# Optimization experiments

Hardware: AMD Instinct MI355X
Metric: run time of the kernel (lower is better)

Reference implementation:

```python
import jax, jax.numpy as jnp
import numpy as np

HEADS = 4
EPS = 1e-12

N_NODES = 50000
N_EDGES = 400000
N_GRAPHS = 512
IN_F = 70
HID = 128
N_LAYERS = 3
N_RELS = 86


def setup_inputs() -> dict:
    key = jax.random.key(0)
    ks = iter(jax.random.split(key, 32))
    inp = {}
    inp['h_x'] = jax.random.normal(next(ks), (N_NODES, IN_F), dtype=jnp.float32)
    inp['h_edge_index'] = jax.random.randint(next(ks), (2, N_EDGES), 0, N_NODES)
    inp['h_batch'] = jnp.sort(jax.random.randint(next(ks), (N_NODES,), 0, N_GRAPHS))
    inp['t_x'] = jax.random.normal(next(ks), (N_NODES, IN_F), dtype=jnp.float32)
    inp['t_edge_index'] = jax.random.randint(next(ks), (2, N_EDGES), 0, N_NODES)
    inp['t_batch'] = jnp.sort(jax.random.randint(next(ks), (N_NODES,), 0, N_GRAPHS))
    inp['rels'] = jax.random.randint(next(ks), (N_GRAPHS,), 0, N_RELS)
    # params
    s = 0.05
    inp['lin0_W'] = jax.random.normal(next(ks), (IN_F, HID), dtype=jnp.float32) * s
    inp['lin0_b'] = jnp.zeros((HID,), dtype=jnp.float32)
    # TransformerConv: lin_query/key/value map HID -> HEADS*HID; lin_skip HID->HID
    inp['Wq'] = jax.random.normal(next(ks), (N_LAYERS, HID, HEADS * HID), dtype=jnp.float32) * s
    inp['bq'] = jnp.zeros((N_LAYERS, HEADS * HID), dtype=jnp.float32)
    inp['Wk'] = jax.random.normal(next(ks), (N_LAYERS, HID, HEADS * HID), dtype=jnp.float32) * s
    inp['bk'] = jnp.zeros((N_LAYERS, HEADS * HID), dtype=jnp.float32)
    inp['Wv'] = jax.random.normal(next(ks), (N_LAYERS, HID, HEADS * HID), dtype=jnp.float32) * s
    inp['bv'] = jnp.zeros((N_LAYERS, HEADS * HID), dtype=jnp.float32)
    inp['Ws'] = jax.random.normal(next(ks), (N_LAYERS, HID, HID), dtype=jnp.float32) * s
    inp['bs'] = jnp.zeros((N_LAYERS, HID), dtype=jnp.float32)
    # cross attention
    inp['wq_W'] = jax.random.normal(next(ks), (HID, HID), dtype=jnp.float32) * s
    inp['wq_b'] = jnp.zeros((HID,), dtype=jnp.float32)
    inp['wk_W'] = jax.random.normal(next(ks), (HID, HID), dtype=jnp.float32) * s
    inp['wk_b'] = jnp.zeros((HID,), dtype=jnp.float32)
    # relation embedding (xavier-ish)
    inp['rel_emb'] = jax.random.normal(next(ks), (N_RELS, HID * HID), dtype=jnp.float32) * (1.0 / np.sqrt(HID))
    return inp


def _transformer_conv(x, src, dst, Wq, bq, Wk, bk, Wv, bv, Ws, bs):
    # PyG TransformerConv, heads=HEADS, concat=False (mean over heads), root skip.
    N = x.shape[0]
    D = Wq.shape[1] // HEADS  # per-head dim = out_channels
    q = (x @ Wq + bq).reshape(N, HEADS, D)
    k = (x @ Wk + bk).reshape(N, HEADS, D)
    v = (x @ Wv + bv).reshape(N, HEADS, D)
    scale = 1.0 / np.sqrt(D).astype(np.float32)
    alpha = jnp.einsum('ehd,ehd->eh', q[dst], k[src]) * scale  # [E,H]
    m = jax.ops.segment_max(alpha, dst, num_segments=N)        # per-dst max
    e = jnp.exp(alpha - m[dst])
    denom = jax.ops.segment_sum(e, dst, num_segments=N)
    a = e / denom[dst]                                          # segment softmax
    out = jax.ops.segment_sum(a[..., None] * v[src], dst, num_segments=N)  # [N,H,D]
    return out.mean(axis=1) + x @ Ws + bs


def _encode(x, edge_index, batch, lin0_W, lin0_b, Wq, bq, Wk, bk, Wv, bv, Ws, bs):
    src, dst = edge_index[0], edge_index[1]
    h = x @ lin0_W + lin0_b  # (dropout is a no-op in eval mode)
    for l in range(N_LAYERS):
        h = jax.nn.relu(_transformer_conv(h, src, dst, Wq[l], bq[l], Wk[l], bk[l], Wv[l], bv[l], Ws[l], bs[l]))
    return jax.ops.segment_sum(h, batch, num_segments=N_GRAPHS)  # global_add_pool [B,HID]


def _normalize(x, axis=-1):
    n = jnp.linalg.norm(x, axis=axis, keepdims=True)
    return x / jnp.maximum(n, EPS)


def reference(h_x, h_edge_index, h_batch, t_x, t_edge_index, t_batch, rels,
              lin0_W, lin0_b, Wq, bq, Wk, bk, Wv, bv, Ws, bs,
              wq_W, wq_b, wk_W, wk_b, rel_emb):
    h_embed = _encode(h_x, h_edge_index, h_batch, lin0_W, lin0_b, Wq, bq, Wk, bk, Wv, bv, Ws, bs)
    t_embed = _encode(t_x, t_edge_index, t_batch, lin0_W, lin0_b, Wq, bq, Wk, bk, Wv, bv, Ws, bs)
    # CrossDrugAttention
    q = h_embed @ wq_W + wq_b
    k = t_embed @ wk_W + wk_b
    interaction = jnp.tanh(q * k)
    # RelationalGeometryWarp
    rel_mat = _normalize(rel_emb[rels].reshape(-1, HID, HID))        # [B,F,F]
    h = _normalize(h_embed + interaction)                            # [B,F]
    t = _normalize(t_embed + interaction)                            # [B,F]
    score = jnp.einsum('bi,bij,bj->b', h, rel_mat, t)
    return score
```

## Files before the change

kernel.cpp:

```cpp
#include <hip/hip_runtime.h>
#include <math.h>

#define HID 128

typedef __attribute__((ext_vector_type(8))) short short8;
typedef __attribute__((ext_vector_type(4))) float f32x4;
typedef __attribute__((ext_vector_type(2))) float f32x2;

__device__ __forceinline__ float bf2f(unsigned int u16) {
  union { unsigned int i; float f; } x; x.i = u16 << 16; return x.f;
}
__device__ __forceinline__ unsigned short f2bf(float f) {
  union { float f; unsigned int i; } x; x.f = f;
  unsigned int i = x.i;
  unsigned int r = i + 0x7FFFu + ((i >> 16) & 1u);
  return (unsigned short)(r >> 16);
}

__device__ __forceinline__ unsigned char f2fp8_sw(float f) {
  union { float f; unsigned int u; } v; v.f = f;
  unsigned int s = (v.u >> 24) & 0x80u;
  v.u &= 0x7FFFFFFFu;
  if (v.f != v.f) return (unsigned char)(s | 0x7Fu);
  if (v.f >= 464.f) return (unsigned char)(s | 0x7Eu);
  if (v.f < 0.0009765625f) return (unsigned char)s;
  int ebits = (int)(v.u >> 23);
  if (ebits >= 121) {
    unsigned int r = v.u + 0x7FFFFu + ((v.u >> 20) & 1u);
    int E = (int)(r >> 23) - 127 + 7;
    unsigned int m = (r >> 20) & 7u;
    if (E >= 16) return (unsigned char)(s | 0x7Eu);
    return (unsigned char)(s | ((unsigned int)E << 3) | m);
  } else {
    int M = (int)rintf(v.f * 512.f);
    if (M > 8) M = 8;
    return (unsigned char)(s | (unsigned int)M);
  }
}

__device__ __forceinline__ unsigned int pack4_fp8(float a, float b, float c, float d) {
#if __has_builtin(__builtin_amdgcn_cvt_pk_fp8_f32)
  int w = 0;
  w = __builtin_amdgcn_cvt_pk_fp8_f32(a, b, w, false);
  w = __builtin_amdgcn_cvt_pk_fp8_f32(c, d, w, true);
  return (unsigned int)w;
#else
  return (unsigned int)f2fp8_sw(a) | ((unsigned int)f2fp8_sw(b) << 8)
       | ((unsigned int)f2fp8_sw(c) << 16) | ((unsigned int)f2fp8_sw(d) << 24);
#endif
}

#if !__has_builtin(__builtin_amdgcn_cvt_pk_f32_fp8)
__device__ __forceinline__ float dec1_fp8(unsigned int u) {
  unsigned int s = (u & 0x80u) << 24;
  unsigned int em = u & 0x7Fu;
  union { unsigned int i; float f; } t;
  t.i = s | ((em << 20) + 0x3C000000u);
  float sub = (float)(int)(u & 7u) * ((u & 0x80u) ? -0.001953125f : 0.001953125f);
  return (em >= 8u) ? t.f : sub;
}
#endif

__device__ __forceinline__ void dec8_fp8(uint2 w, float* o) {
#if __has_builtin(__builtin_amdgcn_cvt_pk_f32_fp8)
  f32x2 p;
  p = __builtin_amdgcn_cvt_pk_f32_fp8((int)w.x, false); o[0] = p.x; o[1] = p.y;
  p = __builtin_amdgcn_cvt_pk_f32_fp8((int)w.x, true);  o[2] = p.x; o[3] = p.y;
  p = __builtin_amdgcn_cvt_pk_f32_fp8((int)w.y, false); o[4] = p.x; o[5] = p.y;
  p = __builtin_amdgcn_cvt_pk_f32_fp8((int)w.y, true);  o[6] = p.x; o[7] = p.y;
#else
  o[0] = dec1_fp8(w.x & 0xFFu);        o[1] = dec1_fp8((w.x >> 8) & 0xFFu);
  o[2] = dec1_fp8((w.x >> 16) & 0xFFu); o[3] = dec1_fp8(w.x >> 24);
  o[4] = dec1_fp8(w.y & 0xFFu);        o[5] = dec1_fp8((w.y >> 8) & 0xFFu);
  o[6] = dec1_fp8((w.y >> 16) & 0xFFu); o[7] = dec1_fp8(w.y >> 24);
#endif
}


__global__ __launch_bounds__(128) void wcvt_kernel(
    const float* __restrict__ Wq, const float* __restrict__ bq,
    const float* __restrict__ Wk, const float* __restrict__ bk,
    const float* __restrict__ Wv, const float* __restrict__ bv,
    const float* __restrict__ Ws, const float* __restrict__ bs,
    unsigned short* __restrict__ BT, float* __restrict__ biascat)
{
  int id = blockIdx.x;
  int l = id / 1664;
  int n = id - l * 1664;
  int k = threadIdx.x;
  const float* W; const float* bias; int nl, ldb;
  if (n < 512)       { W = Wq + (size_t)l * 65536; bias = bq + (size_t)l * 512; nl = n;        ldb = 512; }
  else if (n < 1024) { W = Wk + (size_t)l * 65536; bias = bk + (size_t)l * 512; nl = n - 512;  ldb = 512; }
  else if (n < 1536) { W = Wv + (size_t)l * 65536; bias = bv + (size_t)l * 512; nl = n - 1024; ldb = 512; }
  else               { W = Ws + (size_t)l * 16384; bias = bs + (size_t)l * 128; nl = n - 1536; ldb = 128; }
  size_t dst = (size_t)l * 212992 + (size_t)(n >> 7) * 16384
             + (size_t)((k >> 3) * 128 + (n & 127)) * 8 + (k & 7);
  BT[dst] = f2bf(W[(size_t)k * ldb + nl]);
  if (k == 0) biascat[(size_t)l * 1664 + n] = bias[nl];
}

__global__ __launch_bounds__(256) void lin0_kernel(
    const float* __restrict__ x, const float* __restrict__ W,
    const float* __restrict__ b,
    unsigned short* __restrict__ hb, int N, int inF)
{
  __shared__ float xs[64 * 72];
  const int t = threadIdx.x;
  const int col = t & 127, grp = t >> 7;
  const int n0 = blockIdx.x * 64;
  const int nrows = min(64, N - n0);

  if (inF == 70) {
    const float* xp = x + (size_t)n0 * 70;
    const int r = t >> 2, q = t & 3;
    if (r < nrows) {
      for (int c = q; c < 35; c += 4)
        *(float2*)&xs[r * 72 + c * 2] = *(const float2*)&xp[(size_t)r * 70 + c * 2];
    }
    float w[70];
#pragma unroll
    for (int k = 0; k < 70; k++) w[k] = W[(size_t)k * 128 + col];
    const float bias = b[col];
    __syncthreads();
    for (int i = grp; i < nrows; i += 2) {
      const float* xr = &xs[i * 72];
      float acc = bias;
#pragma unroll
      for (int c = 0; c < 17; c++) {
        f32x4 xv = *(const f32x4*)&xr[c * 4];
        acc = fmaf(xv[0], w[c * 4 + 0], acc);
        acc = fmaf(xv[1], w[c * 4 + 1], acc);
        acc = fmaf(xv[2], w[c * 4 + 2], acc);
        acc = fmaf(xv[3], w[c * 4 + 3], acc);
      }
      acc = fmaf(xr[68], w[68], acc);
      acc = fmaf(xr[69], w[69], acc);
      const int n = n0 + i;
      hb[(size_t)(n >> 7) * 16384 + (size_t)((col >> 3) * 128 + (n & 127)) * 8 + (col & 7)] = f2bf(acc);
    }
  } else {
    const float bias = b[col];
    for (int i = grp; i < nrows; i += 2) {
      const int n = n0 + i;
      float acc = bias;
      for (int k = 0; k < inF; k++) acc += x[(size_t)n * inF + k] * W[(size_t)k * 128 + col];
      hb[(size_t)(n >> 7) * 16384 + (size_t)((col >> 3) * 128 + (n & 127)) * 8 + (col & 7)] = f2bf(acc);
    }
  }
}

__global__ __launch_bounds__(256) void proj_mfma_kernel(
    const unsigned short* __restrict__ A, const unsigned short* __restrict__ BT,
    const float* __restrict__ bias, int M,
    unsigned char* __restrict__ qo, unsigned char* __restrict__ kv,
    unsigned short* __restrict__ sb)
{
  __shared__ unsigned short lsA[8192];
  __shared__ unsigned short lsB[16384];
  __shared__ unsigned int   lsS[2][64 * 35];

  const int t = threadIdx.x;
  const int wv = t >> 6, ln = t & 63;
  const int fr = ln & 15, quad = ln >> 4;
  const int mb = blockIdx.x;
  const int row0 = mb * 64;
  const int panel = mb >> 1, half = mb & 1;

  const unsigned short* Ap = A + (size_t)panel * 16384;

#pragma unroll
  for (int it = 0; it < 4; it++) {
    const int c = it * 256 + t;
    const int Jg = c >> 6, r = c & 63;
    __builtin_amdgcn_global_load_lds(
        (const __attribute__((address_space(1))) void*)(Ap + (size_t)(Jg * 128 + half * 64 + r) * 8),
        (__attribute__((address_space(3))) void*)((char*)lsA + c * 16), 16, 0, 0);
  }

  short8 breg[8];
#pragma unroll
  for (int it = 0; it < 8; it++) {
    const int c = it * 256 + t;
    breg[it] = *(const short8*)(BT + (size_t)c * 8);
  }
  __syncthreads();
#pragma unroll
  for (int it = 0; it < 8; it++) {
    const int c = it * 256 + t;
    *(short8*)((char*)lsB + c * 16) = breg[it];
  }
  __syncthreads();

  for (int nc = 0; nc < 13; nc++) {
    if (nc < 12) {
      const unsigned short* Bn = BT + (size_t)(nc + 1) * 16384;
#pragma unroll
      for (int it = 0; it < 8; it++) {
        const int c = it * 256 + t;
        breg[it] = *(const short8*)(Bn + (size_t)c * 8);
      }
    }

    if (nc > 0) {
      const int pnc = nc - 1;
      const unsigned int* S = lsS[pnc & 1];
      const int pr = pnc >> 2, ncl = pnc & 3;
#pragma unroll
      for (int it = 0; it < 2; it++) {
        const int idx = it * 256 + t;
        const int r = idx >> 3, g = idx & 7;
        const int row = row0 + r;
        if (row < M) {
          uint4 v;
          v.x = S[r * 35 + g * 4 + 0];
          v.y = S[r * 35 + g * 4 + 1];
          v.z = S[r * 35 + g * 4 + 2];
          v.w = S[r * 35 + g * 4 + 3];
          unsigned char* dst = (pr == 0)
              ? qo + (size_t)row * 512 + ncl * 128 + g * 16
              : kv + (size_t)row * 1024 + (pr == 2 ? 512 : 0) + ncl * 128 + g * 16;
          *(uint4*)dst = v;
        }
      }
    }

    f32x4 acc[4][2];
#pragma unroll
    for (int i = 0; i < 4; i++)
#pragma unroll
      for (int j = 0; j < 2; j++) acc[i][j] = (f32x4){0.f, 0.f, 0.f, 0.f};

#pragma unroll
    for (int kb = 0; kb < 4; kb++) {
      short8 af[4], bf[2];
#pragma unroll
      for (int i = 0; i < 4; i++)
        af[i] = *(const short8*)(&lsA[(size_t)((kb * 4 + quad) * 64 + i * 16 + fr) * 8]);
#pragma unroll
      for (int j = 0; j < 2; j++)
        bf[j] = *(const short8*)(&lsB[(size_t)((kb * 4 + quad) * 128 + wv * 32 + j * 16 + fr) * 8]);
#pragma unroll
      for (int i = 0; i < 4; i++)
#pragma unroll
        for (int j = 0; j < 2; j++)
          acc[i][j] = __builtin_amdgcn_mfma_f32_16x16x32_bf16(bf[j], af[i], acc[i][j], 0, 0, 0);
    }

    const int region = nc >> 2;
    if (region < 3) {
      unsigned int* S = lsS[nc & 1];
#pragma unroll
      for (int i = 0; i < 4; i++)
#pragma unroll
        for (int j = 0; j < 2; j++) {
          const int colL = wv * 32 + j * 16 + quad * 4;
          const float4 b4 = *(const float4*)(&bias[nc * 128 + colL]);
          f32x4 c = acc[i][j];
          S[(i * 16 + fr) * 35 + (colL >> 2)] =
              pack4_fp8(c[0] + b4.x, c[1] + b4.y, c[2] + b4.z, c[3] + b4.w);
        }
    } else {
#pragma unroll
      for (int j = 0; j < 2; j++) {
        const int colL = wv * 32 + j * 16 + quad * 4;
        const float4 b4 = *(const float4*)(&bias[nc * 128 + colL]);
#pragma unroll
        for (int i = 0; i < 4; i++) {
          const int row = row0 + i * 16 + fr;
          if (row < M) {
            f32x4 c = acc[i][j];
            uint2 pk;
            pk.x = (unsigned int)f2bf(c[0] + b4.x) | ((unsigned int)f2bf(c[1] + b4.y) << 16);
            pk.y = (unsigned int)f2bf(c[2] + b4.z) | ((unsigned int)f2bf(c[3] + b4.w) << 16);
            *(uint2*)(sb + (size_t)row * 128 + colL) = pk;
          }
        }
      }
    }

    __syncthreads();

    if (nc < 12) {
#pragma unroll
      for (int it = 0; it < 8; it++) {
        const int c = it * 256 + t;
        *(short8*)((char*)lsB + c * 16) = breg[it];
      }
    }
    __syncthreads();
  }
}

__global__ __launch_bounds__(256) void hist_kernel(
    const int* __restrict__ dst, int* __restrict__ deg, int E)
{
  int e = blockIdx.x * 256 + threadIdx.x;
  if (e < E) atomicAdd(&deg[dst[e]], 1);
}

__global__ __launch_bounds__(256) void scan_block_kernel(
    const int* __restrict__ in, int* __restrict__ out, int* __restrict__ bsums, int N)
{
  __shared__ int sm[256];
  int i = blockIdx.x * 256 + threadIdx.x;
  int v = (i < N) ? in[i] : 0;
  sm[threadIdx.x] = v; __syncthreads();
  for (int off = 1; off < 256; off <<= 1) {
    int t = (threadIdx.x >= off) ? sm[threadIdx.x - off] : 0;
    __syncthreads();
    sm[threadIdx.x] += t;
    __syncthreads();
  }
  if (i < N) out[i] = sm[threadIdx.x] - v;
  if (threadIdx.x == 255 && bsums) bsums[blockIdx.x] = sm[255];
}

__global__ __launch_bounds__(256) void scan_finish_kernel(
    int* __restrict__ row_start, int* __restrict__ cursor,
    const int* __restrict__ bsums_scan, int N, int E)
{
  int i = blockIdx.x * 256 + threadIdx.x;
  if (i < N) {
    int val = row_start[i] + bsums_scan[blockIdx.x];
    row_start[i] = val;
    cursor[i] = val;
  }
  if (i == 0) row_start[N] = E;
}

__global__ __launch_bounds__(256) void scatter_kernel(
    const int* __restrict__ src, const int* __restrict__ dst,
    int* __restrict__ cursor, int* __restrict__ csr_src, int E)
{
  int e = blockIdx.x * 256 + threadIdx.x;
  if (e < E) {
    int pos = atomicAdd(&cursor[dst[e]], 1);
    csr_src[pos] = src[e];
  }
}

__global__ __launch_bounds__(256) void node_attn_kernel(
    const unsigned char* __restrict__ q, const unsigned char* __restrict__ kv,
    const int* __restrict__ row_start, const int* __restrict__ csr_src,
    const unsigned short* __restrict__ sb, float* __restrict__ hn,
    unsigned short* __restrict__ hb, int N, int last)
{
  int d = (blockIdx.x * 256 + threadIdx.x) >> 6;
  int lane = threadIdx.x & 63;
  if (d >= N) return;
  int beg = row_start[d], end = row_start[d + 1];

  const float scale = 0.08838834764831845f;
  const uint2 qw = *(const uint2*)(q + (size_t)d * 512 + lane * 8);
  float qd[8];
  dec8_fp8(qw, qd);
#pragma unroll
  for (int j = 0; j < 8; j++) qd[j] *= scale;

  float num[8] = {0.f,0.f,0.f,0.f,0.f,0.f,0.f,0.f};
  float den = 0.f;

  auto krow = [&](int s) { return *(const uint2*)(kv + (size_t)s * 1024 + lane * 8); };
  auto vrow = [&](int s) { return *(const uint2*)(kv + (size_t)s * 1024 + 512 + lane * 8); };
  auto accum = [&](const uint2& kw, const uint2& vw) {
    float kd[8], vd[8];
    dec8_fp8(kw, kd);
    float p = qd[0] * kd[0] + qd[1] * kd[1] + qd[2] * kd[2] + qd[3] * kd[3]
            + qd[4] * kd[4] + qd[5] * kd[5] + qd[6] * kd[6] + qd[7] * kd[7];
    p += __shfl_xor(p, 1);
    p += __shfl_xor(p, 2);
    p += __shfl_xor(p, 4);
    p += __shfl_xor(p, 8);
    float e = __expf(p);
    den += e;
    dec8_fp8(vw, vd);
#pragma unroll
    for (int j = 0; j < 8; j++) num[j] += e * vd[j];
  };

  if (beg < end) {
    const int last_e = end - 1;
    int s0 = csr_src[beg];
    int s1 = csr_src[min(beg + 1, last_e)];
    int s2 = csr_src[min(beg + 2, last_e)];
    uint2 k0 = krow(s0); uint2 v0 = vrow(s0);
    uint2 k1 = krow(s1); uint2 v1 = vrow(s1);
    uint2 k2 = krow(s2); uint2 v2 = vrow(s2);
    for (int i = beg; i < end; i += 3) {
      int t0 = csr_src[min(i + 3, last_e)];
      int t1 = csr_src[min(i + 4, last_e)];
      int t2 = csr_src[min(i + 5, last_e)];
      uint2 ka = krow(t0); uint2 va = vrow(t0);
      uint2 kb = krow(t1); uint2 vb = vrow(t1);
      uint2 kc = krow(t2); uint2 vc = vrow(t2);
      accum(k0, v0);
      if (i + 1 < end) accum(k1, v1);
      if (i + 2 < end) accum(k2, v2);
      k0 = ka; v0 = va; k1 = kb; v1 = vb; k2 = kc; v2 = vc;
    }
  }

  float inv = (den > 0.f) ? 0.25f / den : 0.f;
#pragma unroll
  for (int j = 0; j < 8; j++) {
    float r = num[j] * inv;
    r += __shfl_xor(r, 16);
    r += __shfl_xor(r, 32);
    num[j] = r;
  }
  if (lane < 16) {
    const uint4 sv = *(const uint4*)(sb + (size_t)d * 128 + lane * 8);
    float o[8];
    o[0] = fmaxf(bf2f(sv.x & 0xFFFFu) + num[0], 0.f);
    o[1] = fmaxf(bf2f(sv.x >> 16)     + num[1], 0.f);
    o[2] = fmaxf(bf2f(sv.y & 0xFFFFu) + num[2], 0.f);
    o[3] = fmaxf(bf2f(sv.y >> 16)     + num[3], 0.f);
    o[4] = fmaxf(bf2f(sv.z & 0xFFFFu) + num[4], 0.f);
    o[5] = fmaxf(bf2f(sv.z >> 16)     + num[5], 0.f);
    o[6] = fmaxf(bf2f(sv.w & 0xFFFFu) + num[6], 0.f);
    o[7] = fmaxf(bf2f(sv.w >> 16)     + num[7], 0.f);
    if (last) {
      float* hp = hn + (size_t)d * 128 + lane * 8;
      *(float4*)(hp)     = make_float4(o[0], o[1], o[2], o[3]);
      *(float4*)(hp + 4) = make_float4(o[4], o[5], o[6], o[7]);
    } else {
      uint4 hv;
      hv.x = (unsigned int)f2bf(o[0]) | ((unsigned int)f2bf(o[1]) << 16);
      hv.y = (unsigned int)f2bf(o[2]) | ((unsigned int)f2bf(o[3]) << 16);
      hv.z = (unsigned int)f2bf(o[4]) | ((unsigned int)f2bf(o[5]) << 16);
      hv.w = (unsigned int)f2bf(o[6]) | ((unsigned int)f2bf(o[7]) << 16);
      *(uint4*)(hb + (size_t)(d >> 7) * 16384 + (size_t)(lane * 128 + (d & 127)) * 8) = hv;
    }
  }
}

__global__ __launch_bounds__(128) void pool_kernel(
    const float* __restrict__ h, const int* __restrict__ batch,
    float* __restrict__ emb, int N)
{
  int d = threadIdx.x;
  int n0 = blockIdx.x * 128;
  int n1 = min(n0 + 128, N);
  float acc = 0.f; int cur = -1;
  for (int n = n0; n < n1; n++) {
    int g = batch[n];
    if (g != cur) {
      if (cur >= 0) atomicAdd(&emb[(size_t)cur * 128 + d], acc);
      cur = g; acc = 0.f;
    }
    acc += h[(size_t)n * 128 + d];
  }
  if (cur >= 0) atomicAdd(&emb[(size_t)cur * 128 + d], acc);
}

__global__ __launch_bounds__(128) void score_kernel(
    const float* __restrict__ hemb, const float* __restrict__ temb,
    const int* __restrict__ rels,
    const float* __restrict__ wqW, const float* __restrict__ wqb,
    const float* __restrict__ wkW, const float* __restrict__ wkb,
    const float* __restrict__ rel_emb, float* __restrict__ out)
{
  const int b = blockIdx.x, i = threadIdx.x;
  __shared__ float hs[128], ts[128], hnv[128], tnv[128], red[128];
  hs[i] = hemb[(size_t)b * 128 + i];
  ts[i] = temb[(size_t)b * 128 + i];
  __syncthreads();
  float qv = wqb[i], kv = wkb[i];
  for (int k = 0; k < 128; k++) {
    qv += hs[k] * wqW[k * 128 + i];
    kv += ts[k] * wkW[k * 128 + i];
  }
  float inter = tanhf(qv * kv);
  float hx = hs[i] + inter, tx2 = ts[i] + inter;

  red[i] = hx * hx; __syncthreads();
  for (int s = 64; s > 0; s >>= 1) { if (i < s) red[i] += red[i + s]; __syncthreads(); }
  float hnorm = fmaxf(sqrtf(red[0]), 1e-12f);
  __syncthreads();
  red[i] = tx2 * tx2; __syncthreads();
  for (int s = 64; s > 0; s >>= 1) { if (i < s) red[i] += red[i + s]; __syncthreads(); }
  float tnorm = fmaxf(sqrtf(red[0]), 1e-12f);
  __syncthreads();
  hnv[i] = hx / hnorm; tnv[i] = tx2 / tnorm;
  __syncthreads();

  const float* R = rel_emb + (size_t)rels[b] * 16384 + (size_t)i * 128;
  float dot = 0.f, nrm = 0.f;
  for (int j = 0; j < 128; j++) { float r = R[j]; dot += r * tnv[j]; nrm += r * r; }
  float contrib = hnv[i] * dot / fmaxf(sqrtf(nrm), 1e-12f);
  red[i] = contrib; __syncthreads();
  for (int s = 64; s > 0; s >>= 1) { if (i < s) red[i] += red[i + s]; __syncthreads(); }
  if (i == 0) out[b] = red[0];
}

extern "C" void kernel_launch(void* const* d_in, const int* in_sizes, int n_in,
                              void* d_out, int out_size, void* d_ws, size_t ws_size,
                              hipStream_t stream)
{
  const float* h_x     = (const float*)d_in[0];
  const int*   h_ei    = (const int*)d_in[1];
  const int*   h_batch = (const int*)d_in[2];
  const float* t_x     = (const float*)d_in[3];
  const int*   t_ei    = (const int*)d_in[4];
  const int*   t_batch = (const int*)d_in[5];
  const int*   rels    = (const int*)d_in[6];
  const float* lin0_W  = (const float*)d_in[7];
  const float* lin0_b  = (const float*)d_in[8];
  const float* Wq      = (const float*)d_in[9];
  const float* bq      = (const float*)d_in[10];
  const float* Wk      = (const float*)d_in[11];
  const float* bk      = (const float*)d_in[12];
  const float* Wv      = (const float*)d_in[13];
  const float* bv      = (const float*)d_in[14];
  const float* Ws      = (const float*)d_in[15];
  const float* bs      = (const float*)d_in[16];
  const float* wqW     = (const float*)d_in[17];
  const float* wqb     = (const float*)d_in[18];
  const float* wkW     = (const float*)d_in[19];
  const float* wkb     = (const float*)d_in[20];
  const float* rel_emb = (const float*)d_in[21];

  const int N = in_sizes[2];
  const int E = in_sizes[1] / 2;
  const int G = in_sizes[6];
  const int inF = in_sizes[7] / 128;
  const int nPanels = (N + 127) / 128;
  const int nMB = (N + 63) / 64;

  char* ws = (char*)d_ws;
  size_t off = 0;
  auto alloc = [&](size_t bytes) -> void* {
    void* p = ws + off; off += (bytes + 255) & ~(size_t)255; return p;
  };
  float* hA            = (float*)alloc((size_t)N * 128 * 4);
  unsigned short* hbuf = (unsigned short*)alloc((size_t)nPanels * 16384 * 2);
  unsigned short* sb   = (unsigned short*)alloc((size_t)N * 128 * 2);
  unsigned char* qb    = (unsigned char*)alloc((size_t)N * 512);
  unsigned char* kvbuf = (unsigned char*)alloc((size_t)N * 1024);
  unsigned short* BT   = (unsigned short*)alloc((size_t)3 * 212992 * 2);
  float* biascat       = (float*)alloc((size_t)3 * 1664 * 4);
  int* deg             = (int*)alloc((size_t)(N + 1) * 4);
  int* row_start       = (int*)alloc((size_t)(N + 1) * 4);
  int* cursor          = (int*)alloc((size_t)(N + 1) * 4);
  int* bsums           = (int*)alloc((size_t)1024 * 4);
  int* bsums_scan      = (int*)alloc((size_t)1024 * 4);
  int* csr_src         = (int*)alloc((size_t)E * 4);
  float* hEmb          = (float*)alloc((size_t)G * 128 * 4);
  float* tEmb          = (float*)alloc((size_t)G * 128 * 4);
  (void)ws_size; (void)n_in; (void)out_size;

  const int nScanBlocks = (N + 255) / 256;

  wcvt_kernel<<<3 * 1664, 128, 0, stream>>>(Wq, bq, Wk, bk, Wv, bv, Ws, bs, BT, biascat);

  for (int g = 0; g < 2; g++) {
    const float* x     = g ? t_x : h_x;
    const int*   ei    = g ? t_ei : h_ei;
    const int*   batch = g ? t_batch : h_batch;
    float*       emb   = g ? tEmb : hEmb;
    const int* srcp = ei;
    const int* dstp = ei + E;

    hipMemsetAsync(deg, 0, (size_t)(N + 1) * 4, stream);
    hist_kernel<<<(E + 255) / 256, 256, 0, stream>>>(dstp, deg, E);
    scan_block_kernel<<<nScanBlocks, 256, 0, stream>>>(deg, row_start, bsums, N);
    scan_block_kernel<<<1, 256, 0, stream>>>(bsums, bsums_scan, nullptr, nScanBlocks);
    scan_finish_kernel<<<nScanBlocks, 256, 0, stream>>>(row_start, cursor, bsums_scan, N, E);
    scatter_kernel<<<(E + 255) / 256, 256, 0, stream>>>(srcp, dstp, cursor, csr_src, E);

    lin0_kernel<<<nMB, 256, 0, stream>>>(x, lin0_W, lin0_b, hbuf, N, inF);
    for (int l = 0; l < 3; l++) {
      proj_mfma_kernel<<<nMB, 256, 0, stream>>>(hbuf,
          BT + (size_t)l * 212992, biascat + (size_t)l * 1664, N,
          qb, kvbuf, sb);
      node_attn_kernel<<<(N + 3) / 4, 256, 0, stream>>>(qb, kvbuf,
          row_start, csr_src, sb, hA, hbuf, N, (l == 2) ? 1 : 0);
    }
    hipMemsetAsync(emb, 0, (size_t)G * 128 * 4, stream);
    pool_kernel<<<(N + 127) / 128, 128, 0, stream>>>(hA, batch, emb, N);
  }

  score_kernel<<<G, 128, 0, stream>>>(hEmb, tEmb, rels, wqW, wqb, wkW, wkb,
                                      rel_emb, (float*)d_out);
}
```

Baseline: 1.054 ms.

## Batch head and tail graphs into one combined node set for all kernels

Merges the two drug graphs into a single 2N-node graph with offset indices, so CSR build, lin0, projection, attention and pooling each launch once over twice the work. This halves the kernel launch count and gives each launch more parallelism. The final layer output is also stored as bf16 in the skip buffer instead of fp32, and pooling reads it from there. The price is larger workspace buffers and lower precision in the pooled embeddings.

After: 945.0 us. 10.4% less time.

```diff
diff --git a/kernel.cpp b/kernel.cpp
--- a/kernel.cpp
+++ b/kernel.cpp
@@ -100,22 +100,23 @@
 }
 
 __global__ __launch_bounds__(256) void lin0_kernel(
-    const float* __restrict__ x, const float* __restrict__ W,
-    const float* __restrict__ b,
-    unsigned short* __restrict__ hb, int N, int inF)
+    const float* __restrict__ hx, const float* __restrict__ tx,
+    const float* __restrict__ W, const float* __restrict__ b,
+    unsigned short* __restrict__ hb, int N, int N2, int inF)
 {
   __shared__ float xs[64 * 72];
   const int t = threadIdx.x;
   const int col = t & 127, grp = t >> 7;
   const int n0 = blockIdx.x * 64;
-  const int nrows = min(64, N - n0);
+  const int nrows = min(64, N2 - n0);
 
   if (inF == 70) {
-    const float* xp = x + (size_t)n0 * 70;
     const int r = t >> 2, q = t & 3;
     if (r < nrows) {
+      const int gn = n0 + r;
+      const float* xp = (gn < N) ? (hx + (size_t)gn * 70) : (tx + (size_t)(gn - N) * 70);
       for (int c = q; c < 35; c += 4)
-        *(float2*)&xs[r * 72 + c * 2] = *(const float2*)&xp[(size_t)r * 70 + c * 2];
+        *(float2*)&xs[r * 72 + c * 2] = *(const float2*)&xp[c * 2];
     }
     float w[70];
 #pragma unroll
@@ -142,8 +143,9 @@
     const float bias = b[col];
     for (int i = grp; i < nrows; i += 2) {
       const int n = n0 + i;
+      const float* xp = (n < N) ? (hx + (size_t)n * inF) : (tx + (size_t)(n - N) * inF);
       float acc = bias;
-      for (int k = 0; k < inF; k++) acc += x[(size_t)n * inF + k] * W[(size_t)k * 128 + col];
+      for (int k = 0; k < inF; k++) acc += xp[k] * W[(size_t)k * 128 + col];
       hb[(size_t)(n >> 7) * 16384 + (size_t)((col >> 3) * 128 + (n & 127)) * 8 + (col & 7)] = f2bf(acc);
     }
   }
@@ -291,11 +293,15 @@
   }
 }
 
-__global__ __launch_bounds__(256) void hist_kernel(
-    const int* __restrict__ dst, int* __restrict__ deg, int E)
+__global__ __launch_bounds__(256) void hist2_kernel(
+    const int* __restrict__ hdst, const int* __restrict__ tdst,
+    int* __restrict__ deg, int E, int N)
 {
   int e = blockIdx.x * 256 + threadIdx.x;
-  if (e < E) atomicAdd(&deg[dst[e]], 1);
+  if (e < 2 * E) {
+    int dst = (e < E) ? hdst[e] : (tdst[e - E] + N);
+    atomicAdd(&deg[dst], 1);
+  }
 }
 
 __global__ __launch_bounds__(256) void scan_block_kernel(
@@ -315,39 +321,59 @@
   if (threadIdx.x == 255 && bsums) bsums[blockIdx.x] = sm[255];
 }
 
+__global__ __launch_bounds__(512) void scan_block512_kernel(
+    const int* __restrict__ in, int* __restrict__ out, int N)
+{
+  __shared__ int sm[512];
+  int i = threadIdx.x;
+  int v = (i < N) ? in[i] : 0;
+  sm[i] = v; __syncthreads();
+  for (int off = 1; off < 512; off <<= 1) {
+    int t = (i >= off) ? sm[i - off] : 0;
+    __syncthreads();
+    sm[i] += t;
+    __syncthreads();
+  }
+  if (i < N) out[i] = sm[i] - v;
+}
+
 __global__ __launch_bounds__(256) void scan_finish_kernel(
     int* __restrict__ row_start, int* __restrict__ cursor,
-    const int* __restrict__ bsums_scan, int N, int E)
+    const int* __restrict__ bsums_scan, int N2, int E2)
 {
   int i = blockIdx.x * 256 + threadIdx.x;
-  if (i < N) {
+  if (i < N2) {
     int val = row_start[i] + bsums_scan[blockIdx.x];
     row_start[i] = val;
     cursor[i] = val;
   }
-  if (i == 0) row_start[N] = E;
-}
-
-__global__ __launch_bounds__(256) void scatter_kernel(
-    const int* __restrict__ src, const int* __restrict__ dst,
-    int* __restrict__ cursor, int* __restrict__ csr_src, int E)
+  if (i == 0) row_start[N2] = E2;
+}
+
+__global__ __launch_bounds__(256) void scatter2_kernel(
+    const int* __restrict__ hsrc, const int* __restrict__ hdst,
+    const int* __restrict__ tsrc, const int* __restrict__ tdst,
+    int* __restrict__ cursor, int* __restrict__ csr_src, int E, int N)
 {
   int e = blockIdx.x * 256 + threadIdx.x;
-  if (e < E) {
-    int pos = atomicAdd(&cursor[dst[e]], 1);
-    csr_src[pos] = src[e];
+  if (e < 2 * E) {
+    int src, dst;
+    if (e < E) { src = hsrc[e]; dst = hdst[e]; }
+    else       { src = tsrc[e - E] + N; dst = tdst[e - E] + N; }
+    int pos = atomicAdd(&cursor[dst], 1);
+    csr_src[pos] = src;
   }
 }
 
 __global__ __launch_bounds__(256) void node_attn_kernel(
     const unsigned char* __restrict__ q, const unsigned char* __restrict__ kv,
     const int* __restrict__ row_start, const int* __restrict__ csr_src,
-    const unsigned short* __restrict__ sb, float* __restrict__ hn,
-    unsigned short* __restrict__ hb, int N, int last)
+    unsigned short* __restrict__ sb,
+    unsigned short* __restrict__ hb, int N2, int last)
 {
   int d = (blockIdx.x * 256 + threadIdx.x) >> 6;
   int lane = threadIdx.x & 63;
-  if (d >= N) return;
+  if (d >= N2) return;
   int beg = row_start[d], end = row_start[d + 1];
 
   const float scale = 0.08838834764831845f;
@@ -419,36 +445,35 @@
     o[5] = fmaxf(bf2f(sv.z >> 16)     + num[5], 0.f);
     o[6] = fmaxf(bf2f(sv.w & 0xFFFFu) + num[6], 0.f);
     o[7] = fmaxf(bf2f(sv.w >> 16)     + num[7], 0.f);
+    uint4 hv;
+    hv.x = (unsigned int)f2bf(o[0]) | ((unsigned int)f2bf(o[1]) << 16);
+    hv.y = (unsigned int)f2bf(o[2]) | ((unsigned int)f2bf(o[3]) << 16);
+    hv.z = (unsigned int)f2bf(o[4]) | ((unsigned int)f2bf(o[5]) << 16);
+    hv.w = (unsigned int)f2bf(o[6]) | ((unsigned int)f2bf(o[7]) << 16);
     if (last) {
-      float* hp = hn + (size_t)d * 128 + lane * 8;
-      *(float4*)(hp)     = make_float4(o[0], o[1], o[2], o[3]);
-      *(float4*)(hp + 4) = make_float4(o[4], o[5], o[6], o[7]);
+      *(uint4*)(sb + (size_t)d * 128 + lane * 8) = hv;
     } else {
-      uint4 hv;
-      hv.x = (unsigned int)f2bf(o[0]) | ((unsigned int)f2bf(o[1]) << 16);
-      hv.y = (unsigned int)f2bf(o[2]) | ((unsigned int)f2bf(o[3]) << 16);
-      hv.z = (unsigned int)f2bf(o[4]) | ((unsigned int)f2bf(o[5]) << 16);
-      hv.w = (unsigned int)f2bf(o[6]) | ((unsigned int)f2bf(o[7]) << 16);
       *(uint4*)(hb + (size_t)(d >> 7) * 16384 + (size_t)(lane * 128 + (d & 127)) * 8) = hv;
     }
   }
 }
 
 __global__ __launch_bounds__(128) void pool_kernel(
-    const float* __restrict__ h, const int* __restrict__ batch,
-    float* __restrict__ emb, int N)
+    const unsigned short* __restrict__ sb,
+    const int* __restrict__ hbatch, const int* __restrict__ tbatch,
+    float* __restrict__ emb, int N, int N2, int G)
 {
   int d = threadIdx.x;
   int n0 = blockIdx.x * 128;
-  int n1 = min(n0 + 128, N);
+  int n1 = min(n0 + 128, N2);
   float acc = 0.f; int cur = -1;
   for (int n = n0; n < n1; n++) {
-    int g = batch[n];
+    int g = (n < N) ? hbatch[n] : (tbatch[n - N] + G);
     if (g != cur) {
       if (cur >= 0) atomicAdd(&emb[(size_t)cur * 128 + d], acc);
       cur = g; acc = 0.f;
     }
-    acc += h[(size_t)n * 128 + d];
+    acc += bf2f(sb[(size_t)n * 128 + d]);
   }
   if (cur >= 0) atomicAdd(&emb[(size_t)cur * 128 + d], acc);
 }
@@ -524,62 +549,54 @@
   const int E = in_sizes[1] / 2;
   const int G = in_sizes[6];
   const int inF = in_sizes[7] / 128;
-  const int nPanels = (N + 127) / 128;
-  const int nMB = (N + 63) / 64;
+  const int N2 = 2 * N, E2 = 2 * E;
+  const int nPanels2 = (N2 + 127) / 128;
+  const int nMB2 = (N2 + 63) / 64;
 
   char* ws = (char*)d_ws;
   size_t off = 0;
   auto alloc = [&](size_t bytes) -> void* {
     void* p = ws + off; off += (bytes + 255) & ~(size_t)255; return p;
   };
-  float* hA            = (float*)alloc((size_t)N * 128 * 4);
-  unsigned short* hbuf = (unsigned short*)alloc((size_t)nPanels * 16384 * 2);
-  unsigned short* sb   = (unsigned short*)alloc((size_t)N * 128 * 2);
-  unsigned char* qb    = (unsigned char*)alloc((size_t)N * 512);
-  unsigned char* kvbuf = (unsigned char*)alloc((size_t)N * 1024);
+  unsigned short* hbuf = (unsigned short*)alloc((size_t)nPanels2 * 16384 * 2);
+  unsigned short* sb   = (unsigned short*)alloc((size_t)N2 * 128 * 2);
+  unsigned char* qb    = (unsigned char*)alloc((size_t)N2 * 512);
+  unsigned char* kvbuf = (unsigned char*)alloc((size_t)N2 * 1024);
   unsigned short* BT   = (unsigned short*)alloc((size_t)3 * 212992 * 2);
   float* biascat       = (float*)alloc((size_t)3 * 1664 * 4);
-  int* deg             = (int*)alloc((size_t)(N + 1) * 4);
-  int* row_start       = (int*)alloc((size_t)(N + 1) * 4);
-  int* cursor          = (int*)alloc((size_t)(N + 1) * 4);
+  int* deg             = (int*)alloc((size_t)(N2 + 1) * 4);
+  int* row_start       = (int*)alloc((size_t)(N2 + 1) * 4);
+  int* cursor          = (int*)alloc((size_t)(N2 + 1) * 4);
   int* bsums           = (int*)alloc((size_t)1024 * 4);
   int* bsums_scan      = (int*)alloc((size_t)1024 * 4);
-  int* csr_src         = (int*)alloc((size_t)E * 4);
-  float* hEmb          = (float*)alloc((size_t)G * 128 * 4);
-  float* tEmb          = (float*)alloc((size_t)G * 128 * 4);
+  int* csr_src         = (int*)alloc((size_t)E2 * 4);
+  float* emb           = (float*)alloc((size_t)2 * G * 128 * 4);
   (void)ws_size; (void)n_in; (void)out_size;
 
-  const int nScanBlocks = (N + 255) / 256;
+  const int nScanBlocks = (N2 + 255) / 256;
 
   wcvt_kernel<<<3 * 1664, 128, 0, stream>>>(Wq, bq, Wk, bk, Wv, bv, Ws, bs, BT, biascat);
 
-  for (int g = 0; g < 2; g++) {
-    const float* x     = g ? t_x : h_x;
-    const int*   ei    = g ? t_ei : h_ei;
-    const int*   batch = g ? t_batch : h_batch;
-    float*       emb   = g ? tEmb : hEmb;
-    const int* srcp = ei;
-    const int* dstp = ei + E;
-
-    hipMemsetAsync(deg, 0, (size_t)(N + 1) * 4, stream);
-    hist_kernel<<<(E + 255) / 256, 256, 0, stream>>>(dstp, deg, E);
-    scan_block_kernel<<<nScanBlocks, 256, 0, stream>>>(deg, row_start, bsums, N);
-    scan_block_kernel<<<1, 256, 0, stream>>>(bsums, bsums_scan, nullptr, nScanBlocks);
-    scan_finish_kernel<<<nScanBlocks, 256, 0, stream>>>(row_start, cursor, bsums_scan, N, E);
-    scatter_kernel<<<(E + 255) / 256, 256, 0, stream>>>(srcp, dstp, cursor, csr_src, E);
-
-    lin0_kernel<<<nMB, 256, 0, stream>>>(x, lin0_W, lin0_b, hbuf, N, inF);
-    for (int l = 0; l < 3; l++) {
-      proj_mfma_kernel<<<nMB, 256, 0, stream>>>(hbuf,
-          BT + (size_t)l * 212992, biascat + (size_t)l * 1664, N,
-          qb, kvbuf, sb);
-      node_attn_kernel<<<(N + 3) / 4, 256, 0, stream>>>(qb, kvbuf,
-          row_start, csr_src, sb, hA, hbuf, N, (l == 2) ? 1 : 0);
-    }
-    hipMemsetAsync(emb, 0, (size_t)G * 128 * 4, stream);
-    pool_kernel<<<(N + 127) / 128, 128, 0, stream>>>(hA, batch, emb, N);
-  }
-
-  score_kernel<<<G, 128, 0, stream>>>(hEmb, tEmb, rels, wqW, wqb, wkW, wkb,
-                                      rel_emb, (float*)d_out);
-}
+  hipMemsetAsync(deg, 0, (size_t)(N2 + 1) * 4, stream);
+  hist2_kernel<<<(E2 + 255) / 256, 256, 0, stream>>>(h_ei + E, t_ei + E, deg, E, N);
+  scan_block_kernel<<<nScanBlocks, 256, 0, stream>>>(deg, row_start, bsums, N2);
+  scan_block512_kernel<<<1, 512, 0, stream>>>(bsums, bsums_scan, nScanBlocks);
+  scan_finish_kernel<<<nScanBlocks, 256, 0, stream>>>(row_start, cursor, bsums_scan, N2, E2);
+  scatter2_kernel<<<(E2 + 255) / 256, 256, 0, stream>>>(h_ei, h_ei + E, t_ei, t_ei + E,
+                                                        cursor, csr_src, E, N);
+
+  lin0_kernel<<<nMB2, 256, 0, stream>>>(h_x, t_x, lin0_W, lin0_b, hbuf, N, N2, inF);
+  for (int l = 0; l < 3; l++) {
+    proj_mfma_kernel<<<nMB2, 256, 0, stream>>>(hbuf,
+        BT + (size_t)l * 212992, biascat + (size_t)l * 1664, N2,
+        qb, kvbuf, sb);
+    node_attn_kernel<<<(N2 + 3) / 4, 256, 0, stream>>>(qb, kvbuf,
+        row_start, csr_src, sb, hbuf, N2, (l == 2) ? 1 : 0);
+  }
+
+  hipMemsetAsync(emb, 0, (size_t)2 * G * 128 * 4, stream);
+  pool_kernel<<<(N2 + 127) / 128, 128, 0, stream>>>(sb, h_batch, t_batch, emb, N, N2, G);
+
+  score_kernel<<<G, 128, 0, stream>>>(emb, emb + (size_t)G * 128, rels,
+                                      wqW, wqb, wkW, wkb, rel_emb, (float*)d_out);
+}
```
